# Kernel optimization log

Hardware: AMD Instinct MI355X
Metric: run time of the kernel (lower is better)

Reference implementation:

```python
import jax, jax.numpy as jnp
import numpy as np

N_NODES = 100000
N_EDGES = 400000
D_IN = 128
D_OUT = 128
BN_EPS = 1e-5


def setup_inputs() -> dict:
    key = jax.random.key(0)
    k1, k2, k3, k4, k5 = jax.random.split(key, 5)
    n_feat = jax.random.normal(k1, (N_NODES, D_IN), dtype=jnp.float32)
    edge_index = jax.random.randint(k2, (2, N_EDGES), 0, N_NODES, dtype=jnp.int32)
    edge_weight = jnp.ones((N_EDGES,), dtype=jnp.float32)
    # learned params: BatchNorm1d affine + Linear(in, out, bias=False)
    gamma = jnp.ones((D_IN,), dtype=jnp.float32) + 0.1 * jax.random.normal(k3, (D_IN,), dtype=jnp.float32)
    beta = 0.1 * jax.random.normal(k4, (D_IN,), dtype=jnp.float32)
    W = jax.random.normal(k5, (D_OUT, D_IN), dtype=jnp.float32) * (1.0 / np.sqrt(D_IN))
    return {"n_feat": n_feat, "edge_index": edge_index, "edge_weight": edge_weight,
            "gamma": gamma, "beta": beta, "W": W}


def reference(n_feat, edge_index, edge_weight, gamma, beta, W):
    # BatchNorm1d (training-mode batch stats, biased variance) -> ReLU -> Linear (no bias)
    mu = jnp.mean(n_feat, axis=0)
    var = jnp.mean(jnp.square(n_feat - mu), axis=0)
    xh = (n_feat - mu) * jax.lax.rsqrt(var + BN_EPS)
    y = jax.nn.relu(gamma * xh + beta)
    h = y @ W.T  # [N, D_OUT]
    # sparse adjacency matmul: out[row] += w * h[col]
    row, col = edge_index[0], edge_index[1]
    msgs = h[col] * edge_weight[:, None]          # gather, [E, D_OUT]
    agg = jax.ops.segment_sum(msgs, row, num_segments=N_NODES)
    return h * h + agg
```

## Files before the change

### kernel.cpp

```cpp
#include <hip/hip_runtime.h>

#define N_NODES 100000
#define N_EDGES 400000
#define D 128
#define BN_EPS 1e-5f
#define ELL_CAP 32

#define NSTAT 64
#define CS_BLOCKS 625
#define CS_ITER 20

#define WS_STATS   0
#define WS_HB      (NSTAT * 256)
#define WS_DEG2    (WS_HB + N_NODES * D / 2)
#define WS_ELL2    (WS_DEG2 + N_NODES)
#define WS_ELL2_END (WS_ELL2 + N_NODES * ELL_CAP * 2)
#define WS_SCALE   (NSTAT * 256)
#define WS_SHIFT   (WS_SCALE + 128)
#define WS_WT      (WS_SHIFT + 128)
#define WS_H       (WS_WT + D * D)
#define WS_DEG     (WS_H + N_NODES * D)
#define WS_ROWPTR  (WS_DEG + N_NODES)
#define WS_CURSOR  (WS_ROWPTR + N_NODES + 1)
#define WS_CSRCOL  (WS_CURSOR + N_NODES)
#define WS_CSRW    (WS_CSRCOL + N_EDGES)
#define WS_END     (WS_CSRW + N_EDGES)

typedef __attribute__((ext_vector_type(8))) short short8;
typedef __attribute__((ext_vector_type(4))) float f32x4;

static __device__ __forceinline__ unsigned short f2bf(float f) {
    union { float f; unsigned u; } v; v.f = f;
    unsigned r = v.u + 0x7FFF + ((v.u >> 16) & 1);
    return (unsigned short)(r >> 16);
}
static __device__ __forceinline__ float bf2f(unsigned short b) {
    union { unsigned u; float f; } v; v.u = ((unsigned)b) << 16;
    return v.f;
}

__global__ __launch_bounds__(256) void colstats_kernel(const float* __restrict__ x,
                                                       float* __restrict__ stats,
                                                       int* __restrict__ deg) {
    int tid = blockIdx.x * 256 + threadIdx.x;
    if (deg && tid < N_NODES) deg[tid] = 0;
    const int NTH = CS_BLOCKS * 256;
    const float4* x4 = (const float4*)x;
    float4 v[CS_ITER];
    #pragma unroll
    for (int i = 0; i < CS_ITER; i++) v[i] = x4[tid + i * NTH];
    float4 s = {0.f, 0.f, 0.f, 0.f};
    float4 q = {0.f, 0.f, 0.f, 0.f};
    #pragma unroll
    for (int i = 0; i < CS_ITER; i++) {
        s.x += v[i].x; s.y += v[i].y; s.z += v[i].z; s.w += v[i].w;
        q.x += v[i].x * v[i].x; q.y += v[i].y * v[i].y;
        q.z += v[i].z * v[i].z; q.w += v[i].w * v[i].w;
    }

    __shared__ float4 ss[256];
    __shared__ float4 sq[256];
    ss[threadIdx.x] = s;
    sq[threadIdx.x] = q;
    __syncthreads();
    if (threadIdx.x < 32) {
        float4 a = ss[threadIdx.x];
        float4 b = sq[threadIdx.x];
        for (int i = 32; i < 256; i += 32) {
            float4 t1 = ss[threadIdx.x + i];
            float4 t2 = sq[threadIdx.x + i];
            a.x += t1.x; a.y += t1.y; a.z += t1.z; a.w += t1.w;
            b.x += t2.x; b.y += t2.y; b.z += t2.z; b.w += t2.w;
        }
        float* st = stats + (blockIdx.x % NSTAT) * 256;
        int colb = (threadIdx.x * 4) & 127;
        atomicAdd(&st[colb + 0], a.x);
        atomicAdd(&st[colb + 1], a.y);
        atomicAdd(&st[colb + 2], a.z);
        atomicAdd(&st[colb + 3], a.w);
        atomicAdd(&st[128 + colb + 0], b.x);
        atomicAdd(&st[128 + colb + 1], b.y);
        atomicAdd(&st[128 + colb + 2], b.z);
        atomicAdd(&st[128 + colb + 3], b.w);
    }
}

__global__ __launch_bounds__(256) void fill_ell2_kernel(const int* __restrict__ ei,
                                                        const float* __restrict__ ew,
                                                        int* __restrict__ deg,
                                                        int2* __restrict__ ell2) {
    int e = blockIdx.x * 256 + threadIdx.x;
    if (e >= N_EDGES) return;
    int r = ei[e];
    int c = ei[N_EDGES + e];
    float w = ew[e];
    int slot = atomicAdd(&deg[r], 1);
    if (slot < ELL_CAP) ell2[r * ELL_CAP + slot] = make_int2(c, __float_as_int(w));
}

#define YPAD 136
#define OPAD 132
__global__ __launch_bounds__(256) void gemm_mfma2_kernel(const float* __restrict__ x,
                                                         const float* __restrict__ stats,
                                                         const float* __restrict__ gamma,
                                                         const float* __restrict__ beta,
                                                         const float* __restrict__ W,
                                                         unsigned short* __restrict__ hb,
                                                         float* __restrict__ out) {
    __shared__ __align__(16) unsigned char smem[52224];
    __shared__ float sscale[128];
    __shared__ float sshift[128];
    unsigned short* Wl = (unsigned short*)smem;
    unsigned short* Yl = (unsigned short*)(smem + 128 * YPAD * 2);
    float* Outs = (float*)smem;

    int t = threadIdx.x;
    int row0 = blockIdx.x * 64;

    if (t < 128) {
        float sum = 0.f, sq = 0.f;
        #pragma unroll 16
        for (int c = 0; c < NSTAT; c++) {
            sum += stats[c * 256 + t];
            sq  += stats[c * 256 + 128 + t];
        }
        float mu  = sum * (1.0f / N_NODES);
        float var = sq * (1.0f / N_NODES) - mu * mu;
        float sc  = gamma[t] * rsqrtf(var + BN_EPS);
        sscale[t] = sc;
        sshift[t] = beta[t] - mu * sc;
    }
    __syncthreads();

    for (int i = t; i < 2048; i += 256) {
        int n  = i >> 4;
        int k8 = (i & 15) * 8;
        float4 w0 = *(const float4*)(W + n * 128 + k8);
        float4 w1 = *(const float4*)(W + n * 128 + k8 + 4);
        short8 p;
        p[0] = (short)f2bf(w0.x); p[1] = (short)f2bf(w0.y);
        p[2] = (short)f2bf(w0.z); p[3] = (short)f2bf(w0.w);
        p[4] = (short)f2bf(w1.x); p[5] = (short)f2bf(w1.y);
        p[6] = (short)f2bf(w1.z); p[7] = (short)f2bf(w1.w);
        *(short8*)(Wl + n * YPAD + k8) = p;
    }
    for (int i = t; i < 64 * 32; i += 256) {
        int r  = i >> 5;
        int c4 = (i & 31) * 4;
        int grow = row0 + r;
        int srow = grow < N_NODES ? grow : N_NODES - 1;
        float4 v = *(const float4*)(x + (size_t)srow * D + c4);
        float a0 = fmaxf(fmaf(v.x, sscale[c4 + 0], sshift[c4 + 0]), 0.f);
        float a1 = fmaxf(fmaf(v.y, sscale[c4 + 1], sshift[c4 + 1]), 0.f);
        float a2 = fmaxf(fmaf(v.z, sscale[c4 + 2], sshift[c4 + 2]), 0.f);
        float a3 = fmaxf(fmaf(v.w, sscale[c4 + 3], sshift[c4 + 3]), 0.f);
        ushort4 b;
        b.x = f2bf(a0); b.y = f2bf(a1); b.z = f2bf(a2); b.w = f2bf(a3);
        *(ushort4*)(Yl + r * YPAD + c4) = b;
    }
    __syncthreads();

    int lane = t & 63;
    int wave = t >> 6;
    int m16  = lane & 15;
    int quad = lane >> 4;
    int wrow0 = wave * 16;

    f32x4 acc[8];
    #pragma unroll
    for (int nt = 0; nt < 8; nt++) acc[nt] = (f32x4){0.f, 0.f, 0.f, 0.f};

    #pragma unroll
    for (int kc = 0; kc < 4; kc++) {
        short8 a = *(const short8*)(Yl + (wrow0 + m16) * YPAD + kc * 32 + quad * 8);
        #pragma unroll
        for (int nt = 0; nt < 8; nt++) {
            short8 b = *(const short8*)(Wl + (nt * 16 + m16) * YPAD + kc * 32 + quad * 8);
            acc[nt] = __builtin_amdgcn_mfma_f32_16x16x32_bf16(a, b, acc[nt], 0, 0, 0);
        }
    }
    __syncthreads();

    #pragma unroll
    for (int nt = 0; nt < 8; nt++) {
        #pragma unroll
        for (int r = 0; r < 4; r++) {
            Outs[(wrow0 + quad * 4 + r) * OPAD + nt * 16 + m16] = acc[nt][r];
        }
    }
    __syncthreads();

    for (int i = t; i < 64 * 32; i += 256) {
        int r  = i >> 5;
        int c4 = (i & 31) * 4;
        int grow = row0 + r;
        if (grow < N_NODES) {
            float4 v = *(const float4*)(Outs + r * OPAD + c4);
            ushort4 hb4;
            hb4.x = f2bf(v.x); hb4.y = f2bf(v.y); hb4.z = f2bf(v.z); hb4.w = f2bf(v.w);
            *(ushort4*)(hb + (size_t)grow * D + c4) = hb4;
            float4 sq = {v.x * v.x, v.y * v.y, v.z * v.z, v.w * v.w};
            *(float4*)(out + (size_t)grow * D + c4) = sq;
        }
    }
}

__global__ __launch_bounds__(256) void gather_ell2_kernel(const int* __restrict__ deg,
                                                          const int2* __restrict__ ell2,
                                                          const unsigned short* __restrict__ hb,
                                                          float* __restrict__ out) {
    int lane = threadIdx.x & 15;
    int n = blockIdx.x * 16 + (threadIdx.x >> 4);
    if (n >= N_NODES) return;
    int dg = deg[n];
    if (dg > ELL_CAP) dg = ELL_CAP;
    int dg16 = dg < 16 ? dg : 16;

    int2 my = make_int2(0, 0);
    if (lane < dg16) my = ell2[n * ELL_CAP + lane];

    float acc[8] = {0.f, 0.f, 0.f, 0.f, 0.f, 0.f, 0.f, 0.f};
    int s = 0;
    for (; s + 4 <= dg16; s += 4) {
        int   c0 = __shfl(my.x, s + 0, 16); float w0 = __int_as_float(__shfl(my.y, s + 0, 16));
        int   c1 = __shfl(my.x, s + 1, 16); float w1 = __int_as_float(__shfl(my.y, s + 1, 16));
        int   c2 = __shfl(my.x, s + 2, 16); float w2 = __int_as_float(__shfl(my.y, s + 2, 16));
        int   c3 = __shfl(my.x, s + 3, 16); float w3 = __int_as_float(__shfl(my.y, s + 3, 16));
        short8 v0 = *(const short8*)(hb + (size_t)c0 * D + lane * 8);
        short8 v1 = *(const short8*)(hb + (size_t)c1 * D + lane * 8);
        short8 v2 = *(const short8*)(hb + (size_t)c2 * D + lane * 8);
        short8 v3 = *(const short8*)(hb + (size_t)c3 * D + lane * 8);
        #pragma unroll
        for (int j = 0; j < 8; j++) {
            acc[j] = fmaf(w0, bf2f((unsigned short)v0[j]), acc[j]);
            acc[j] = fmaf(w1, bf2f((unsigned short)v1[j]), acc[j]);
            acc[j] = fmaf(w2, bf2f((unsigned short)v2[j]), acc[j]);
            acc[j] = fmaf(w3, bf2f((unsigned short)v3[j]), acc[j]);
        }
    }
    for (; s < dg16; s++) {
        int c = __shfl(my.x, s, 16);
        float w = __int_as_float(__shfl(my.y, s, 16));
        short8 v = *(const short8*)(hb + (size_t)c * D + lane * 8);
        #pragma unroll
        for (int j = 0; j < 8; j++) acc[j] = fmaf(w, bf2f((unsigned short)v[j]), acc[j]);
    }
    for (s = 16; s < dg; s++) {
        int2 cw = ell2[n * ELL_CAP + s];
        float w = __int_as_float(cw.y);
        short8 v = *(const short8*)(hb + (size_t)cw.x * D + lane * 8);
        #pragma unroll
        for (int j = 0; j < 8; j++) acc[j] = fmaf(w, bf2f((unsigned short)v[j]), acc[j]);
    }

    float* o = out + (size_t)n * D + lane * 8;
    float4 a = *(const float4*)o;
    float4 b = *(const float4*)(o + 4);
    a.x += acc[0]; a.y += acc[1]; a.z += acc[2]; a.w += acc[3];
    b.x += acc[4]; b.y += acc[5]; b.z += acc[6]; b.w += acc[7];
    *(float4*)o = a;
    *(float4*)(o + 4) = b;
}

__global__ __launch_bounds__(128) void finalize_kernel(const float* __restrict__ stats,
                                                       const float* __restrict__ gamma,
                                                       const float* __restrict__ beta,
                                                       float* __restrict__ scale,
                                                       float* __restrict__ shift) {
    int d = threadIdx.x;
    float sum = 0.f, sq = 0.f;
    #pragma unroll 16
    for (int c = 0; c < NSTAT; c++) {
        sum += stats[c * 256 + d];
        sq  += stats[c * 256 + 128 + d];
    }
    float mu  = sum * (1.0f / N_NODES);
    float var = sq * (1.0f / N_NODES) - mu * mu;
    float sc  = gamma[d] * rsqrtf(var + BN_EPS);
    scale[d] = sc;
    shift[d] = beta[d] - mu * sc;
}

__global__ __launch_bounds__(256) void transposeW_kernel(const float* __restrict__ W,
                                                         float* __restrict__ Wt) {
    int i = blockIdx.x * blockDim.x + threadIdx.x;
    if (i < D * D) {
        int j = i >> 7;
        int k = i & 127;
        Wt[k * D + j] = W[i];
    }
}

template <int WRITE_SQ>
__global__ __launch_bounds__(256) void gemm_kernel(const float* __restrict__ x,
                                                   const float* __restrict__ scale,
                                                   const float* __restrict__ shift,
                                                   const float* __restrict__ Wt,
                                                   float* __restrict__ h,
                                                   float* __restrict__ out) {
    __shared__ float Ws[D * D];
    __shared__ float Ys[32 * D];
    int t = threadIdx.x;
    const float4* Wt4 = (const float4*)Wt;
    float4* Ws4 = (float4*)Ws;
    #pragma unroll 4
    for (int i = t; i < D * D / 4; i += 256) Ws4[i] = Wt4[i];
    int row0 = blockIdx.x * 32;
    const float4* x4 = (const float4*)(x + (size_t)row0 * D);
    float4* Ys4 = (float4*)Ys;
    #pragma unroll 2
    for (int i = t; i < 32 * D / 4; i += 256) {
        int c4 = (i & 31) * 4;
        float4 v = x4[i];
        v.x = fmaxf(fmaf(v.x, scale[c4 + 0], shift[c4 + 0]), 0.f);
        v.y = fmaxf(fmaf(v.y, scale[c4 + 1], shift[c4 + 1]), 0.f);
        v.z = fmaxf(fmaf(v.z, scale[c4 + 2], shift[c4 + 2]), 0.f);
        v.w = fmaxf(fmaf(v.w, scale[c4 + 3], shift[c4 + 3]), 0.f);
        Ys4[i] = v;
    }
    __syncthreads();
    int cg = t & 31;
    int rg = t >> 5;
    float4 acc[4] = {{0,0,0,0},{0,0,0,0},{0,0,0,0},{0,0,0,0}};
    #pragma unroll 2
    for (int k = 0; k < D; k += 4) {
        float4 w0 = *(const float4*)&Ws[(k + 0) * D + cg * 4];
        float4 w1 = *(const float4*)&Ws[(k + 1) * D + cg * 4];
        float4 w2 = *(const float4*)&Ws[(k + 2) * D + cg * 4];
        float4 w3 = *(const float4*)&Ws[(k + 3) * D + cg * 4];
        #pragma unroll
        for (int r = 0; r < 4; r++) {
            float4 y = *(const float4*)&Ys[(rg * 4 + r) * D + k];
            acc[r].x = fmaf(y.x, w0.x, fmaf(y.y, w1.x, fmaf(y.z, w2.x, fmaf(y.w, w3.x, acc[r].x))));
            acc[r].y = fmaf(y.x, w0.y, fmaf(y.y, w1.y, fmaf(y.z, w2.y, fmaf(y.w, w3.y, acc[r].y))));
            acc[r].z = fmaf(y.x, w0.z, fmaf(y.y, w1.z, fmaf(y.z, w2.z, fmaf(y.w, w3.z, acc[r].z))));
            acc[r].w = fmaf(y.x, w0.w, fmaf(y.y, w1.w, fmaf(y.z, w2.w, fmaf(y.w, w3.w, acc[r].w))));
        }
    }
    #pragma unroll
    for (int r = 0; r < 4; r++) {
        size_t row = (size_t)row0 + rg * 4 + r;
        float4 v = acc[r];
        *(float4*)&h[row * D + cg * 4] = v;
        if (WRITE_SQ) {
            float4 sqv = {v.x * v.x, v.y * v.y, v.z * v.z, v.w * v.w};
            *(float4*)&out[row * D + cg * 4] = sqv;
        }
    }
}

__global__ __launch_bounds__(256) void hist_kernel(const int* __restrict__ ei,
                                                   int* __restrict__ deg) {
    int e = blockIdx.x * 256 + threadIdx.x;
    if (e < N_EDGES) atomicAdd(&deg[ei[e]], 1);
}

__global__ __launch_bounds__(1024) void scan_kernel(const int* __restrict__ deg,
                                                    int* __restrict__ row_ptr,
                                                    int* __restrict__ cursor) {
    __shared__ int part[1024];
    int t = threadIdx.x;
    const int CHUNK = 100;
    int base = t * CHUNK;
    int s = 0;
    if (base < N_NODES) {
        for (int i = 0; i < CHUNK; i++) s += deg[base + i];
    }
    part[t] = s;
    __syncthreads();
    for (int off = 1; off < 1024; off <<= 1) {
        int v = (t >= off) ? part[t - off] : 0;
        __syncthreads();
        part[t] += v;
        __syncthreads();
    }
    int pre = (t == 0) ? 0 : part[t - 1];
    if (base < N_NODES) {
        for (int i = 0; i < CHUNK; i++) {
            row_ptr[base + i] = pre;
            cursor[base + i] = pre;
            pre += deg[base + i];
        }
    }
    if (t == 1023) row_ptr[N_NODES] = part[1023];
}

__global__ __launch_bounds__(256) void fill_kernel(const int* __restrict__ ei,
                                                   const float* __restrict__ ew,
                                                   int* __restrict__ cursor,
                                                   int* __restrict__ csr_col,
                                                   float* __restrict__ csr_w) {
    int e = blockIdx.x * 256 + threadIdx.x;
    if (e >= N_EDGES) return;
    int r = ei[e];
    int c = ei[N_EDGES + e];
    int slot = atomicAdd(&cursor[r], 1);
    csr_col[slot] = c;
    csr_w[slot] = ew[e];
}

__global__ __launch_bounds__(256) void gather_kernel(const int* __restrict__ row_ptr,
                                                     const int* __restrict__ csr_col,
                                                     const float* __restrict__ csr_w,
                                                     const float* __restrict__ h,
                                                     float* __restrict__ out) {
    int lane = threadIdx.x & 31;
    int n = blockIdx.x * 8 + (threadIdx.x >> 5);
    if (n >= N_NODES) return;
    int s0 = row_ptr[n];
    int s1 = row_ptr[n + 1];
    float4 acc = {0.f, 0.f, 0.f, 0.f};
    for (int s = s0; s < s1; s++) {
        int c = csr_col[s];
        float w = csr_w[s];
        float4 v = *(const float4*)&h[(size_t)c * D + lane * 4];
        acc.x = fmaf(w, v.x, acc.x);
        acc.y = fmaf(w, v.y, acc.y);
        acc.z = fmaf(w, v.z, acc.z);
        acc.w = fmaf(w, v.w, acc.w);
    }
    float4 hv = *(const float4*)&h[(size_t)n * D + lane * 4];
    float4 o;
    o.x = fmaf(hv.x, hv.x, acc.x);
    o.y = fmaf(hv.y, hv.y, acc.y);
    o.z = fmaf(hv.z, hv.z, acc.z);
    o.w = fmaf(hv.w, hv.w, acc.w);
    *(float4*)&out[(size_t)n * D + lane * 4] = o;
}

__global__ __launch_bounds__(256) void scatter_kernel(const int* __restrict__ ei,
                                                      const float* __restrict__ ew,
                                                      const float* __restrict__ h,
                                                      float* __restrict__ out) {
    int lane = threadIdx.x & 31;
    int e = blockIdx.x * 8 + (threadIdx.x >> 5);
    if (e >= N_EDGES) return;
    int r = ei[e];
    int c = ei[N_EDGES + e];
    float w = ew[e];
    float4 v = *(const float4*)&h[(size_t)c * D + lane * 4];
    float* o = out + (size_t)r * D + lane * 4;
    atomicAdd(o + 0, v.x * w);
    atomicAdd(o + 1, v.y * w);
    atomicAdd(o + 2, v.z * w);
    atomicAdd(o + 3, v.w * w);
}

extern "C" void kernel_launch(void* const* d_in, const int* in_sizes, int n_in,
                              void* d_out, int out_size, void* d_ws, size_t ws_size,
                              hipStream_t stream) {
    const float* n_feat = (const float*)d_in[0];
    const int*   ei     = (const int*)d_in[1];
    const float* ew     = (const float*)d_in[2];
    const float* gamma  = (const float*)d_in[3];
    const float* beta   = (const float*)d_in[4];
    const float* W      = (const float*)d_in[5];
    float* out = (float*)d_out;

    float* ws    = (float*)d_ws;
    float* stats = ws + WS_STATS;

    bool ell_ok = ws_size >= (size_t)WS_ELL2_END * sizeof(float);
    bool csr_ok = ws_size >= (size_t)WS_END * sizeof(float);

    hipMemsetAsync(stats, 0, NSTAT * 256 * sizeof(float), stream);

    if (ell_ok) {
        unsigned short* hb  = (unsigned short*)(ws + WS_HB);
        int*  deg  = (int*)ws + WS_DEG2;
        int2* ell2 = (int2*)((int*)ws + WS_ELL2);

        colstats_kernel<<<CS_BLOCKS, 256, 0, stream>>>(n_feat, stats, deg);
        fill_ell2_kernel<<<(N_EDGES + 255) / 256, 256, 0, stream>>>(ei, ew, deg, ell2);
        gemm_mfma2_kernel<<<(N_NODES + 63) / 64, 256, 0, stream>>>(n_feat, stats, gamma, beta, W, hb, out);
        gather_ell2_kernel<<<(N_NODES + 15) / 16, 256, 0, stream>>>(deg, ell2, hb, out);
    } else if (csr_ok) {
        float* scale = ws + WS_SCALE;
        float* shift = ws + WS_SHIFT;
        float* Wt    = ws + WS_WT;
        float* h     = ws + WS_H;
        int*   deg     = (int*)ws + WS_DEG;
        int*   row_ptr = (int*)ws + WS_ROWPTR;
        int*   cursor  = (int*)ws + WS_CURSOR;
        int*   csr_col = (int*)ws + WS_CSRCOL;
        float* csr_w   = ws + WS_CSRW;

        colstats_kernel<<<CS_BLOCKS, 256, 0, stream>>>(n_feat, stats, nullptr);
        finalize_kernel<<<1, 128, 0, stream>>>(stats, gamma, beta, scale, shift);
        transposeW_kernel<<<64, 256, 0, stream>>>(W, Wt);
        hipMemsetAsync(deg, 0, N_NODES * sizeof(int), stream);
        gemm_kernel<0><<<N_NODES / 32, 256, 0, stream>>>(n_feat, scale, shift, Wt, h, out);
        hist_kernel<<<(N_EDGES + 255) / 256, 256, 0, stream>>>(ei, deg);
        scan_kernel<<<1, 1024, 0, stream>>>(deg, row_ptr, cursor);
        fill_kernel<<<(N_EDGES + 255) / 256, 256, 0, stream>>>(ei, ew, cursor, csr_col, csr_w);
        gather_kernel<<<(N_NODES + 7) / 8, 256, 0, stream>>>(row_ptr, csr_col, csr_w, h, out);
    } else {
        float* scale = ws + WS_SCALE;
        float* shift = ws + WS_SHIFT;
        float* Wt    = ws + WS_WT;
        float* h     = ws + WS_H;
        colstats_kernel<<<CS_BLOCKS, 256, 0, stream>>>(n_feat, stats, nullptr);
        finalize_kernel<<<1, 128, 0, stream>>>(stats, gamma, beta, scale, shift);
        transposeW_kernel<<<64, 256, 0, stream>>>(W, Wt);
        gemm_kernel<1><<<N_NODES / 32, 256, 0, stream>>>(n_feat, scale, shift, Wt, h, out);
        scatter_kernel<<<(N_EDGES + 7) / 8, 256, 0, stream>>>(ei, ew, h, out);
    }
}
```

Before: 201.4 us.

## Precompute bf16 W and BN scale/shift once, slim GEMM kernel LDS usage

Adds a small kernel that converts W to bf16 and computes the BN scale and shift once, instead of every GEMM block redoing the stats reduction and W conversion. The GEMM now keeps only the activation tile in LDS and reads W operands straight from global memory/cache, which allows more blocks per CU. It also writes results directly from the MFMA accumulators, dropping the LDS staging and two barriers. The cost is an extra launch plus narrower scalar stores (2-byte and 4-byte, strided per lane) instead of vectorized rows.

```diff
diff --git a/kernel.cpp b/kernel.cpp
--- a/kernel.cpp
+++ b/kernel.cpp
@@ -15,6 +15,10 @@
 #define WS_DEG2    (WS_HB + N_NODES * D / 2)
 #define WS_ELL2    (WS_DEG2 + N_NODES)
 #define WS_ELL2_END (WS_ELL2 + N_NODES * ELL_CAP * 2)
+#define WS_WB      WS_ELL2_END
+#define WS_SCL     (WS_WB + 8192)
+#define WS_SHF     (WS_SCL + 128)
+#define WS_ELL_END2 (WS_SHF + 128)
 #define WS_SCALE   (NSTAT * 256)
 #define WS_SHIFT   (WS_SCALE + 128)
 #define WS_WT      (WS_SHIFT + 128)
@@ -98,26 +102,22 @@
     if (slot < ELL_CAP) ell2[r * ELL_CAP + slot] = make_int2(c, __float_as_int(w));
 }
 
-#define YPAD 136
-#define OPAD 132
-__global__ __launch_bounds__(256) void gemm_mfma2_kernel(const float* __restrict__ x,
-                                                         const float* __restrict__ stats,
-                                                         const float* __restrict__ gamma,
-                                                         const float* __restrict__ beta,
-                                                         const float* __restrict__ W,
-                                                         unsigned short* __restrict__ hb,
-                                                         float* __restrict__ out) {
-    __shared__ __align__(16) unsigned char smem[52224];
-    __shared__ float sscale[128];
-    __shared__ float sshift[128];
-    unsigned short* Wl = (unsigned short*)smem;
-    unsigned short* Yl = (unsigned short*)(smem + 128 * YPAD * 2);
-    float* Outs = (float*)smem;
-
+__global__ __launch_bounds__(256) void convw_finalize_kernel(const float* __restrict__ W,
+                                                             const float* __restrict__ stats,
+                                                             const float* __restrict__ gamma,
+                                                             const float* __restrict__ beta,
+                                                             unsigned short* __restrict__ Wb,
+                                                             float* __restrict__ scale,
+                                                             float* __restrict__ shift) {
+    int b = blockIdx.x;
     int t = threadIdx.x;
-    int row0 = blockIdx.x * 64;
-
-    if (t < 128) {
+    if (b < 16) {
+        int i = b * 256 + t;
+        float4 v = *(const float4*)(W + i * 4);
+        ushort4 o;
+        o.x = f2bf(v.x); o.y = f2bf(v.y); o.z = f2bf(v.z); o.w = f2bf(v.w);
+        *(ushort4*)(Wb + i * 4) = o;
+    } else if (t < 128) {
         float sum = 0.f, sq = 0.f;
         #pragma unroll 16
         for (int c = 0; c < NSTAT; c++) {
@@ -127,36 +127,40 @@
         float mu  = sum * (1.0f / N_NODES);
         float var = sq * (1.0f / N_NODES) - mu * mu;
         float sc  = gamma[t] * rsqrtf(var + BN_EPS);
-        sscale[t] = sc;
-        sshift[t] = beta[t] - mu * sc;
-    }
-    __syncthreads();
-
-    for (int i = t; i < 2048; i += 256) {
-        int n  = i >> 4;
-        int k8 = (i & 15) * 8;
-        float4 w0 = *(const float4*)(W + n * 128 + k8);
-        float4 w1 = *(const float4*)(W + n * 128 + k8 + 4);
-        short8 p;
-        p[0] = (short)f2bf(w0.x); p[1] = (short)f2bf(w0.y);
-        p[2] = (short)f2bf(w0.z); p[3] = (short)f2bf(w0.w);
-        p[4] = (short)f2bf(w1.x); p[5] = (short)f2bf(w1.y);
-        p[6] = (short)f2bf(w1.z); p[7] = (short)f2bf(w1.w);
-        *(short8*)(Wl + n * YPAD + k8) = p;
-    }
-    for (int i = t; i < 64 * 32; i += 256) {
-        int r  = i >> 5;
-        int c4 = (i & 31) * 4;
-        int grow = row0 + r;
-        int srow = grow < N_NODES ? grow : N_NODES - 1;
-        float4 v = *(const float4*)(x + (size_t)srow * D + c4);
-        float a0 = fmaxf(fmaf(v.x, sscale[c4 + 0], sshift[c4 + 0]), 0.f);
-        float a1 = fmaxf(fmaf(v.y, sscale[c4 + 1], sshift[c4 + 1]), 0.f);
-        float a2 = fmaxf(fmaf(v.z, sscale[c4 + 2], sshift[c4 + 2]), 0.f);
-        float a3 = fmaxf(fmaf(v.w, sscale[c4 + 3], sshift[c4 + 3]), 0.f);
-        ushort4 b;
-        b.x = f2bf(a0); b.y = f2bf(a1); b.z = f2bf(a2); b.w = f2bf(a3);
-        *(ushort4*)(Yl + r * YPAD + c4) = b;
+        scale[t] = sc;
+        shift[t] = beta[t] - mu * sc;
+    }
+}
+
+#define YPAD 136
+__global__ __launch_bounds__(256, 4) void gemm_mfma3_kernel(const float* __restrict__ x,
+                                                            const float* __restrict__ scale,
+                                                            const float* __restrict__ shift,
+                                                            const unsigned short* __restrict__ Wb,
+                                                            unsigned short* __restrict__ hb,
+                                                            float* __restrict__ out) {
+    __shared__ __align__(16) unsigned short Yl[64 * YPAD];
+    int t = threadIdx.x;
+    int row0 = blockIdx.x * 64;
+
+    {
+        int c4 = (t & 31) * 4;
+        float4 sc = *(const float4*)(scale + c4);
+        float4 sh = *(const float4*)(shift + c4);
+        #pragma unroll
+        for (int p = 0; p < 8; p++) {
+            int i = t + p * 256;
+            int r = i >> 5;
+            int grow = row0 + r;
+            int srow = grow < N_NODES ? grow : N_NODES - 1;
+            float4 v = *(const float4*)(x + (size_t)srow * D + c4);
+            ushort4 y;
+            y.x = f2bf(fmaxf(fmaf(v.x, sc.x, sh.x), 0.f));
+            y.y = f2bf(fmaxf(fmaf(v.y, sc.y, sh.y), 0.f));
+            y.z = f2bf(fmaxf(fmaf(v.z, sc.z, sh.z), 0.f));
+            y.w = f2bf(fmaxf(fmaf(v.w, sc.w, sh.w), 0.f));
+            *(ushort4*)(Yl + r * YPAD + c4) = y;
+        }
     }
     __syncthreads();
 
@@ -170,37 +174,30 @@
     #pragma unroll
     for (int nt = 0; nt < 8; nt++) acc[nt] = (f32x4){0.f, 0.f, 0.f, 0.f};
 
+    const unsigned short* wb = Wb + m16 * D + quad * 8;
+    const unsigned short* yl = Yl + (wrow0 + m16) * YPAD + quad * 8;
     #pragma unroll
     for (int kc = 0; kc < 4; kc++) {
-        short8 a = *(const short8*)(Yl + (wrow0 + m16) * YPAD + kc * 32 + quad * 8);
+        short8 a = *(const short8*)(yl + kc * 32);
         #pragma unroll
         for (int nt = 0; nt < 8; nt++) {
-            short8 b = *(const short8*)(Wl + (nt * 16 + m16) * YPAD + kc * 32 + quad * 8);
+            short8 b = *(const short8*)(wb + nt * 16 * D + kc * 32);
             acc[nt] = __builtin_amdgcn_mfma_f32_16x16x32_bf16(a, b, acc[nt], 0, 0, 0);
         }
     }
-    __syncthreads();
 
     #pragma unroll
-    for (int nt = 0; nt < 8; nt++) {
-        #pragma unroll
-        for (int r = 0; r < 4; r++) {
-            Outs[(wrow0 + quad * 4 + r) * OPAD + nt * 16 + m16] = acc[nt][r];
-        }
-    }
-    __syncthreads();
-
-    for (int i = t; i < 64 * 32; i += 256) {
-        int r  = i >> 5;
-        int c4 = (i & 31) * 4;
-        int grow = row0 + r;
+    for (int r = 0; r < 4; r++) {
+        int grow = row0 + wrow0 + quad * 4 + r;
         if (grow < N_NODES) {
-            float4 v = *(const float4*)(Outs + r * OPAD + c4);
-            ushort4 hb4;
-            hb4.x = f2bf(v.x); hb4.y = f2bf(v.y); hb4.z = f2bf(v.z); hb4.w = f2bf(v.w);
-            *(ushort4*)(hb + (size_t)grow * D + c4) = hb4;
-            float4 sq = {v.x * v.x, v.y * v.y, v.z * v.z, v.w * v.w};
-            *(float4*)(out + (size_t)grow * D + c4) = sq;
+            float* orow = out + (size_t)grow * D + m16;
+            unsigned short* hrow = hb + (size_t)grow * D + m16;
+            #pragma unroll
+            for (int nt = 0; nt < 8; nt++) {
+                float v = acc[nt][r];
+                orow[nt * 16] = v * v;
+                hrow[nt * 16] = f2bf(v);
+            }
         }
     }
 }
@@ -460,7 +457,7 @@
     float* ws    = (float*)d_ws;
     float* stats = ws + WS_STATS;
 
-    bool ell_ok = ws_size >= (size_t)WS_ELL2_END * sizeof(float);
+    bool ell_ok = ws_size >= (size_t)WS_ELL_END2 * sizeof(float);
     bool csr_ok = ws_size >= (size_t)WS_END * sizeof(float);
 
     hipMemsetAsync(stats, 0, NSTAT * 256 * sizeof(float), stream);
@@ -469,10 +466,14 @@
         unsigned short* hb  = (unsigned short*)(ws + WS_HB);
         int*  deg  = (int*)ws + WS_DEG2;
         int2* ell2 = (int2*)((int*)ws + WS_ELL2);
+        unsigned short* Wb = (unsigned short*)(ws + WS_WB);
+        float* scl = ws + WS_SCL;
+        float* shf = ws + WS_SHF;
 
         colstats_kernel<<<CS_BLOCKS, 256, 0, stream>>>(n_feat, stats, deg);
         fill_ell2_kernel<<<(N_EDGES + 255) / 256, 256, 0, stream>>>(ei, ew, deg, ell2);
-        gemm_mfma2_kernel<<<(N_NODES + 63) / 64, 256, 0, stream>>>(n_feat, stats, gamma, beta, W, hb, out);
+        convw_finalize_kernel<<<17, 256, 0, stream>>>(W, stats, gamma, beta, Wb, scl, shf);
+        gemm_mfma3_kernel<<<(N_NODES + 63) / 64, 256, 0, stream>>>(n_feat, scl, shf, Wb, hb, out);
         gather_ell2_kernel<<<(N_NODES + 15) / 16, 256, 0, stream>>>(deg, ell2, hb, out);
     } else if (csr_ok) {
         float* scale = ws + WS_SCALE;
```

Result: no change. 201.9 us (+0.3%).
